# Kernel tuning notes

Measured on AMD Instinct MI355X. Metric: run time of the kernel, lower is better.

The kernel has to match this reference:

```python
import jax, jax.numpy as jnp
import numpy as np
import math

N_HEADS, INPUT_DIM, EMBED_DIM = 8, 512, 512
KEY_DIM = EMBED_DIM // N_HEADS  # val_dim == key_dim == 64
B, NQ, G = 4, 2048, 2048


def setup_inputs() -> dict:
    key = jax.random.key(0)
    ks = jax.random.split(key, 7)
    stdv_k = 1.0 / math.sqrt(KEY_DIM)
    stdv_e = 1.0 / math.sqrt(EMBED_DIM)
    return {
        "q": jax.random.normal(ks[0], (B, NQ, INPUT_DIM), jnp.float32),
        "h": jax.random.normal(ks[1], (B, G, INPUT_DIM), jnp.float32),
        "mask": jax.random.randint(ks[2], (B, NQ, G), 0, 2) == 1,  # True = attention not possible
        "W_query": jax.random.uniform(ks[3], (N_HEADS, INPUT_DIM, KEY_DIM), jnp.float32, -stdv_k, stdv_k),
        "W_key": jax.random.uniform(ks[4], (N_HEADS, INPUT_DIM, KEY_DIM), jnp.float32, -stdv_k, stdv_k),
        "W_val": jax.random.uniform(ks[5], (N_HEADS, INPUT_DIM, KEY_DIM), jnp.float32, -stdv_k, stdv_k),
        "W_out": jax.random.uniform(ks[6], (N_HEADS, KEY_DIM, EMBED_DIM), jnp.float32, -stdv_e, stdv_e),
    }


def reference(q, h, mask, W_query, W_key, W_val, W_out):
    norm = 1.0 / math.sqrt(KEY_DIM)
    # Per-head projections: (H, B, S, kd)
    Q = jnp.einsum("bqd,hdk->hbqk", q, W_query)
    K = jnp.einsum("bgd,hdk->hbgk", h, W_key)
    V = jnp.einsum("bgd,hdv->hbgv", h, W_val)
    # Full attention scores: (H, B, NQ, G)
    comp = norm * jnp.einsum("hbqk,hbgk->hbqg", Q, K)
    m = mask[None]  # (1, B, NQ, G) broadcasts over heads
    comp = jnp.where(m, -jnp.inf, comp)
    attn = jax.nn.softmax(comp, axis=-1)
    attn = jnp.where(m, 0.0, attn)  # mirrors the clone + zero step (also fixes all-masked rows)
    heads = jnp.einsum("hbqg,hbgv->hbqv", attn, V)
    # Output projection: flatten heads and apply W_out (H, vd, E)
    out = jnp.einsum("hbqv,hve->bqe", heads, W_out)
    return out
```

## Files before the change

### kernel.cpp

```cpp
#include <hip/hip_runtime.h>
#include <hip/hip_bf16.h>
#include <stdint.h>

#define NHEADS 8
#define INDIM 512
#define EMB 512
#define BSZ 4
#define NQS 2048
#define GS 2048

#define ALPHA_F 0.18033688011112042f

#if __has_builtin(__builtin_amdgcn_exp2f)
#define EXP2(x) __builtin_amdgcn_exp2f(x)
#else
#define EXP2(x) __expf((x)*0.69314718056f)
#endif

typedef short bf16x8 __attribute__((ext_vector_type(8)));
typedef float f32x4 __attribute__((ext_vector_type(4)));
typedef float f32x16 __attribute__((ext_vector_type(16)));
typedef unsigned int u32x4 __attribute__((ext_vector_type(4)));

static __device__ __forceinline__ unsigned short f2bf(float f) {
  unsigned int u = __builtin_bit_cast(unsigned int, f);
  unsigned int rounding = 0x7FFFu + ((u >> 16) & 1u);
  u += rounding;
  return (unsigned short)(u >> 16);
}

typedef __attribute__((address_space(3))) void lds_void;
typedef __attribute__((address_space(1))) const void gm_void;
static __device__ __forceinline__ void gll16(const void* g, void* s) {
  __builtin_amdgcn_global_load_lds((gm_void*)g, (lds_void*)s, 16, 0, 0);
}

__global__ void k_prep(const float4* __restrict__ q, const float4* __restrict__ h,
                       const void* __restrict__ mask,
                       const float* __restrict__ wq, const float* __restrict__ wk,
                       const float* __restrict__ wv, const float* __restrict__ wo,
                       ushort4* __restrict__ qb, ushort4* __restrict__ hb,
                       unsigned short* __restrict__ wqt, unsigned short* __restrict__ wkvt,
                       unsigned short* __restrict__ wot, unsigned short* __restrict__ maskB16) {
  int blk = blockIdx.x, t = threadIdx.x;
  if (blk < 2048) {
    const float4* src = blk < 1024 ? q : h;
    ushort4* dst = blk < 1024 ? qb : hb;
    int base = (blk & 1023) * 256 + t;
#pragma unroll
    for (int i = 0; i < 4; i++) {
      int idx = base + i * 262144;
      float4 v = src[idx];
      ushort4 o;
      o.x = f2bf(v.x); o.y = f2bf(v.y); o.z = f2bf(v.z); o.w = f2bf(v.w);
      dst[idx] = o;
    }
  } else if (blk < 3072) {
    const unsigned int* m32h = (const unsigned int*)mask;
    bool bytes = __ballot(m32h[t & 63] > 1u) != 0ull;
    int base = (blk - 2048) * 256 + t;
#pragma unroll
    for (int i = 0; i < 4; i++) {
      int widx = base + i * 262144;
      unsigned int bits = 0;
      if (bytes) {
        const uchar4* p = (const uchar4*)((const unsigned char*)mask + (size_t)widx * 16);
#pragma unroll
        for (int j = 0; j < 4; j++) {
          uchar4 v = p[j];
          bits |= ((v.x ? 1u : 0u) << (4 * j)) | ((v.y ? 1u : 0u) << (4 * j + 1)) |
                  ((v.z ? 1u : 0u) << (4 * j + 2)) | ((v.w ? 1u : 0u) << (4 * j + 3));
        }
      } else {
        const int4* p = (const int4*)((const int*)mask + (size_t)widx * 16);
#pragma unroll
        for (int j = 0; j < 4; j++) {
          int4 v = p[j];
          bits |= ((v.x ? 1u : 0u) << (4 * j)) | ((v.y ? 1u : 0u) << (4 * j + 1)) |
                  ((v.z ? 1u : 0u) << (4 * j + 2)) | ((v.w ? 1u : 0u) << (4 * j + 3));
        }
      }
      maskB16[widx] = (unsigned short)bits;
    }
  } else {
    int id = (blk - 3072) * 256 + t;
#pragma unroll
    for (int i = 0; i < 8; i++) {
      int e = id * 8 + i;
      int which = e >> 18, r = e & 262143;
      int k = r & 511, n = r >> 9;
      int hh = n >> 6, j = n & 63;
      if (which == 0) wqt[r] = f2bf(wq[hh * 32768 + k * 64 + j] * ALPHA_F);
      else if (which == 1) wkvt[r] = f2bf(wk[hh * 32768 + k * 64 + j]);
      else if (which == 2) wkvt[262144 + r] = f2bf(wv[hh * 32768 + k * 64 + j]);
      else wot[r] = f2bf(wo[k * 512 + n]);
    }
  }
}

template <int MODE>
__global__ __launch_bounds__(256) void k_gemm3(const unsigned short* __restrict__ A,
                                               const unsigned short* __restrict__ Bt,
                                               void* __restrict__ C, void* __restrict__ C2) {
  __shared__ unsigned short As[2][4096];
  __shared__ unsigned short Bs[2][8192];
  int m0 = blockIdx.x * 64, n0 = blockIdx.y * 128;
  int t = threadIdx.x;
  int w = t >> 6, l = t & 63, c = l & 15, lg = l >> 4;
  int wr = w >> 1, wc = w & 1;

  int rbA = t >> 7, kcc = (t >> 4) & 7, cc = t & 15;
  const unsigned short* aG = A + (size_t)(m0 + rbA * 16 + cc) * 512 + kcc * 8;
  const unsigned short* bG = Bt + (size_t)(n0 + rbA * 16 + cc) * 512 + kcc * 8;
  int ldsOff = w * 1024 + (t & 63) * 16;

  f32x4 acc[2][4];
#pragma unroll
  for (int mi = 0; mi < 2; mi++)
#pragma unroll
    for (int ni = 0; ni < 4; ni++) acc[mi][ni] = {0.f, 0.f, 0.f, 0.f};

  gll16(aG, (char*)As[0] + ldsOff);
  gll16(aG + 32 * 512, (char*)As[0] + ldsOff + 4096);
  gll16(bG, (char*)Bs[0] + ldsOff);
  gll16(bG + 32 * 512, (char*)Bs[0] + ldsOff + 4096);
  gll16(bG + 64 * 512, (char*)Bs[0] + ldsOff + 8192);
  gll16(bG + 96 * 512, (char*)Bs[0] + ldsOff + 12288);

  for (int kk = 0; kk < 8; kk++) {
    int cur = kk & 1;
    asm volatile("s_waitcnt vmcnt(0)" ::: "memory");
    __builtin_amdgcn_s_barrier();
    if (kk < 7) {
      int ko = (kk + 1) * 64;
      gll16(aG + ko, (char*)As[cur ^ 1] + ldsOff);
      gll16(aG + ko + 32 * 512, (char*)As[cur ^ 1] + ldsOff + 4096);
      gll16(bG + ko, (char*)Bs[cur ^ 1] + ldsOff);
      gll16(bG + ko + 32 * 512, (char*)Bs[cur ^ 1] + ldsOff + 4096);
      gll16(bG + ko + 64 * 512, (char*)Bs[cur ^ 1] + ldsOff + 8192);
      gll16(bG + ko + 96 * 512, (char*)Bs[cur ^ 1] + ldsOff + 12288);
    }
    bf16x8 af[2][2], bfr[4][2];
#pragma unroll
    for (int kc = 0; kc < 2; kc++) {
#pragma unroll
      for (int mi = 0; mi < 2; mi++)
        af[mi][kc] = *(const bf16x8*)((const char*)As[cur] + ((wr * 2 + mi) * 128 + (kc * 4 + lg) * 16 + c) * 16);
#pragma unroll
      for (int ni = 0; ni < 4; ni++)
        bfr[ni][kc] = *(const bf16x8*)((const char*)Bs[cur] + ((wc * 4 + ni) * 128 + (kc * 4 + lg) * 16 + c) * 16);
    }
#pragma unroll
    for (int kc = 0; kc < 2; kc++)
#pragma unroll
      for (int mi = 0; mi < 2; mi++)
#pragma unroll
        for (int ni = 0; ni < 4; ni++)
          acc[mi][ni] = __builtin_amdgcn_mfma_f32_16x16x32_bf16(af[mi][kc], bfr[ni][kc], acc[mi][ni], 0, 0, 0);
  }

#pragma unroll
  for (int mi = 0; mi < 2; mi++)
#pragma unroll
    for (int ni = 0; ni < 4; ni++) {
      int row = m0 + wr * 32 + mi * 16 + 4 * lg;
      int col = n0 + wc * 64 + ni * 16 + c;
#pragma unroll
      for (int r = 0; r < 4; r++)
        ((float*)C)[(size_t)(row + r) * 512 + col] = acc[mi][ni][r];
    }
}

__global__ __launch_bounds__(256) void k_gemmQKV2(const unsigned short* __restrict__ qb_,
                                                  const unsigned short* __restrict__ hb_,
                                                  const unsigned short* __restrict__ wqt,
                                                  const unsigned short* __restrict__ wkvt,
                                                  unsigned short* __restrict__ Qp,
                                                  unsigned short* __restrict__ Kp,
                                                  unsigned short* __restrict__ Vt) {
  __shared__ unsigned short As[2][4096];
  __shared__ unsigned short Bs[2][4096];
  int ny = blockIdx.y;
  const unsigned short* A = (ny < 4) ? qb_ : hb_;
  const unsigned short* Bt = (ny < 4) ? wqt : wkvt;
  int n0 = (ny < 4) ? ny * 128 : (ny - 4) * 128;
  int m0 = blockIdx.x * 128;
  int t = threadIdx.x;
  int w = t >> 6, l = t & 63, c = l & 15, lg = l >> 4;
  int wr = w >> 1, wc = w & 1;

  int sRow = (t >> 6) * 16 + (t & 15);
  int sK = ((t >> 4) & 3) * 8;
  const unsigned short* aG = A + (size_t)(m0 + sRow) * 512 + sK;
  const unsigned short* bG = Bt + (size_t)(n0 + sRow) * 512 + sK;
  int ldsOff = t * 16;

  f32x4 acc[4][4];
#pragma unroll
  for (int mi = 0; mi < 4; mi++)
#pragma unroll
    for (int ni = 0; ni < 4; ni++) acc[mi][ni] = {0.f, 0.f, 0.f, 0.f};

  gll16(aG, (char*)As[0] + ldsOff);
  gll16(aG + 64 * 512, (char*)As[0] + ldsOff + 4096);
  gll16(bG, (char*)Bs[0] + ldsOff);
  gll16(bG + 64 * 512, (char*)Bs[0] + ldsOff + 4096);

  for (int kk = 0; kk < 16; kk++) {
    int cur = kk & 1;
    asm volatile("s_waitcnt vmcnt(0)" ::: "memory");
    __builtin_amdgcn_s_barrier();
    if (kk < 15) {
      int ko = (kk + 1) * 32;
      gll16(aG + ko, (char*)As[cur ^ 1] + ldsOff);
      gll16(aG + ko + 64 * 512, (char*)As[cur ^ 1] + ldsOff + 4096);
      gll16(bG + ko, (char*)Bs[cur ^ 1] + ldsOff);
      gll16(bG + ko + 64 * 512, (char*)Bs[cur ^ 1] + ldsOff + 4096);
    }
    bf16x8 af[4], bfr[4];
#pragma unroll
    for (int mi = 0; mi < 4; mi++)
      af[mi] = *(const bf16x8*)((const char*)As[cur] + (((wr * 4 + mi) * 64 + l) * 16));
#pragma unroll
    for (int ni = 0; ni < 4; ni++)
      bfr[ni] = *(const bf16x8*)((const char*)Bs[cur] + (((wc * 4 + ni) * 64 + l) * 16));
#pragma unroll
    for (int mi = 0; mi < 4; mi++)
#pragma unroll
      for (int ni = 0; ni < 4; ni++)
        acc[mi][ni] = __builtin_amdgcn_mfma_f32_16x16x32_bf16(af[mi], bfr[ni], acc[mi][ni], 0, 0, 0);
  }

#pragma unroll
  for (int mi = 0; mi < 4; mi++)
#pragma unroll
    for (int ni = 0; ni < 4; ni++) {
      int row = m0 + wr * 64 + mi * 16 + 4 * lg;
      int col = n0 + wc * 64 + ni * 16 + c;
      if (ny < 4) {
#pragma unroll
        for (int r = 0; r < 4; r++)
          Qp[(size_t)(row + r) * 512 + col] = f2bf(acc[mi][ni][r]);
      } else if (col < 512) {
#pragma unroll
        for (int r = 0; r < 4; r++)
          Kp[(size_t)(row + r) * 512 + col] = f2bf(acc[mi][ni][r]);
      } else {
        int col5 = col - 512, hd2 = col5 >> 6, vv = col5 & 63;
        int bb = row >> 11, g = row & 2047;
        ushort4 u;
        u.x = f2bf(acc[mi][ni][0]);
        u.y = f2bf(acc[mi][ni][1]);
        u.z = f2bf(acc[mi][ni][2]);
        u.w = f2bf(acc[mi][ni][3]);
        *(ushort4*)(Vt + (size_t)((bb * 8 + hd2) * 64 + vv) * GS + g) = u;
      }
    }
}

__global__ __launch_bounds__(256, 2) void k_attn8(const unsigned short* __restrict__ Qp,
                                                  const unsigned short* __restrict__ Kp,
                                                  const unsigned short* __restrict__ Vt,
                                                  const unsigned short* __restrict__ maskB16,
                                                  unsigned short* __restrict__ Hd) {
  __shared__ unsigned short Ksh[2][4096];
  __shared__ unsigned short Vsh[2][4096];

  int bid = blockIdx.x;
  int fid = (bid & 7) * 64 + (bid >> 3);
  int qtile = fid & 15;
  int bh = fid >> 4;
  int b = bh >> 3, hd = bh & 7;

  int t = threadIdx.x;
  int w = t >> 6, l = t & 63;
  int lo = l & 31, hi = l >> 5, hi4 = hi * 4;
  int q = qtile * 128 + w * 32 + lo;

  const unsigned short* qrow = Qp + (size_t)(b * NQS + q) * 512 + hd * 64 + hi * 8;
  bf16x8 qf[4];
#pragma unroll
  for (int s = 0; s < 4; s++) qf[s] = *(const bf16x8*)(qrow + s * 16);

  const unsigned short* kg0 = Kp + (size_t)(b * GS + lo) * 512 + hd * 64 + w * 16 + hi * 8;
  int vbS = (t >> 7) & 1, s2S = (t >> 6) & 1;
  const unsigned short* vg0 = Vt + (size_t)(bh * 64 + vbS * 32 + lo) * GS + s2S * 16 + hi * 8;
  char* kd[2] = {(char*)Ksh[0] + w * 1024, (char*)Ksh[1] + w * 1024};
  char* vd[2] = {(char*)Vsh[0] + w * 1024, (char*)Vsh[1] + w * 1024};

  f32x16 o0, o1;
#pragma unroll
  for (int i = 0; i < 16; i++) { o0[i] = 0.f; o1[i] = 0.f; }
  float ls[4] = {0.f, 0.f, 0.f, 0.f};

  const unsigned long long* mrow = (const unsigned long long*)maskB16 + (size_t)(b * NQS + q) * 32;

  gll16(kg0, kd[0]);
  gll16(kg0 + 32 * 512, kd[0] + 4096);
  gll16(vg0, vd[0]);
  gll16(vg0 + 32, vd[0] + 4096);
  unsigned long long wm = mrow[0], wmn = 0;

  for (int kt = 0; kt < 32; kt++) {
    int cur = kt & 1;
    asm volatile("s_waitcnt vmcnt(0)" ::: "memory");
    __builtin_amdgcn_s_barrier();
    if (kt < 31) {
      const unsigned short* kg = kg0 + (size_t)(kt + 1) * 64 * 512;
      const unsigned short* vg = vg0 + (size_t)(kt + 1) * 64;
      gll16(kg, kd[cur ^ 1]);
      gll16(kg + 32 * 512, kd[cur ^ 1] + 4096);
      gll16(vg, vd[cur ^ 1]);
      gll16(vg + 32, vd[cur ^ 1] + 4096);
      wmn = mrow[kt + 1];
    }

#pragma unroll
    for (int g2 = 0; g2 < 2; g2++) {
      const unsigned short* Kc = (const unsigned short*)Ksh[cur] + g2 * 2048;
      f32x16 sreg;
#pragma unroll
      for (int i = 0; i < 16; i++) sreg[i] = 0.f;
      __builtin_amdgcn_s_setprio(1);
#pragma unroll
      for (int s = 0; s < 4; s++) {
        bf16x8 ka = *(const bf16x8*)(Kc + (s * 64 + l) * 8);
        sreg = __builtin_amdgcn_mfma_f32_32x32x16_bf16(ka, qf[s], sreg, 0, 0, 0);
      }
      __builtin_amdgcn_s_setprio(0);
      unsigned int mbits = (unsigned int)(wm >> (g2 * 32));
      float p[16];
#pragma unroll
      for (int r = 0; r < 16; r++) {
        float e = EXP2(sreg[r]);
        unsigned bit = (mbits >> ((r & 3) + 8 * (r >> 2) + hi4)) & 1u;
        p[r] = bit ? 0.f : e;
        ls[r & 3] += p[r];
      }
      unsigned int cw0, cw1, cw2, cw3, cw4, cw5, cw6, cw7;
      asm("v_cvt_pk_bf16_f32 %0, %1, %2" : "=v"(cw0) : "v"(p[0]), "v"(p[1]));
      asm("v_cvt_pk_bf16_f32 %0, %1, %2" : "=v"(cw1) : "v"(p[2]), "v"(p[3]));
      asm("v_cvt_pk_bf16_f32 %0, %1, %2" : "=v"(cw2) : "v"(p[4]), "v"(p[5]));
      asm("v_cvt_pk_bf16_f32 %0, %1, %2" : "=v"(cw3) : "v"(p[6]), "v"(p[7]));
      asm("v_cvt_pk_bf16_f32 %0, %1, %2" : "=v"(cw4) : "v"(p[8]), "v"(p[9]));
      asm("v_cvt_pk_bf16_f32 %0, %1, %2" : "=v"(cw5) : "v"(p[10]), "v"(p[11]));
      asm("v_cvt_pk_bf16_f32 %0, %1, %2" : "=v"(cw6) : "v"(p[12]), "v"(p[13]));
      asm("v_cvt_pk_bf16_f32 %0, %1, %2" : "=v"(cw7) : "v"(p[14]), "v"(p[15]));
      asm("v_permlane32_swap_b32 %0, %1" : "+v"(cw0), "+v"(cw2));
      asm("v_permlane32_swap_b32 %0, %1" : "+v"(cw1), "+v"(cw3));
      asm("v_permlane32_swap_b32 %0, %1" : "+v"(cw4), "+v"(cw6));
      asm("v_permlane32_swap_b32 %0, %1" : "+v"(cw5), "+v"(cw7));
      u32x4 pw0 = {cw0, cw1, cw2, cw3};
      u32x4 pw1 = {cw4, cw5, cw6, cw7};
      bf16x8 pb0 = __builtin_bit_cast(bf16x8, pw0);
      bf16x8 pb1 = __builtin_bit_cast(bf16x8, pw1);
      const unsigned short* Vc = (const unsigned short*)Vsh[cur] + g2 * 2048;
      bf16x8 va00 = *(const bf16x8*)(Vc + (0 * 64 + l) * 8);
      bf16x8 va01 = *(const bf16x8*)(Vc + (1 * 64 + l) * 8);
      bf16x8 va10 = *(const bf16x8*)(Vc + (2 * 64 + l) * 8);
      bf16x8 va11 = *(const bf16x8*)(Vc + (3 * 64 + l) * 8);
      __builtin_amdgcn_s_setprio(1);
      o0 = __builtin_amdgcn_mfma_f32_32x32x16_bf16(va00, pb0, o0, 0, 0, 0);
      o1 = __builtin_amdgcn_mfma_f32_32x32x16_bf16(va10, pb0, o1, 0, 0, 0);
      o0 = __builtin_amdgcn_mfma_f32_32x32x16_bf16(va01, pb1, o0, 0, 0, 0);
      o1 = __builtin_amdgcn_mfma_f32_32x32x16_bf16(va11, pb1, o1, 0, 0, 0);
      __builtin_amdgcn_s_setprio(0);
    }
    wm = wmn;
  }

  float lsum = (ls[0] + ls[1]) + (ls[2] + ls[3]);
  lsum += __shfl_xor(lsum, 32);
  float inv = lsum > 0.f ? 1.0f / lsum : 0.f;
  unsigned short* hrow = Hd + (size_t)(b * NQS + q) * 512 + hd * 64;
#pragma unroll
  for (int vt = 0; vt < 2; vt++) {
#pragma unroll
    for (int gr = 0; gr < 4; gr++) {
      ushort4 u;
      float v0 = (vt ? o1[gr * 4 + 0] : o0[gr * 4 + 0]) * inv;
      float v1 = (vt ? o1[gr * 4 + 1] : o0[gr * 4 + 1]) * inv;
      float v2 = (vt ? o1[gr * 4 + 2] : o0[gr * 4 + 2]) * inv;
      float v3 = (vt ? o1[gr * 4 + 3] : o0[gr * 4 + 3]) * inv;
      u.x = f2bf(v0); u.y = f2bf(v1); u.z = f2bf(v2); u.w = f2bf(v3);
      int vv = vt * 32 + 8 * gr + hi4;
      *(ushort4*)(hrow + vv) = u;
    }
  }
}


extern "C" void kernel_launch(void* const* d_in, const int* in_sizes, int n_in,
                              void* d_out, int out_size, void* d_ws, size_t ws_size,
                              hipStream_t stream) {
  const float* q = (const float*)d_in[0];
  const float* h = (const float*)d_in[1];
  const void* mask = d_in[2];
  const float* wq = (const float*)d_in[3];
  const float* wk = (const float*)d_in[4];
  const float* wv = (const float*)d_in[5];
  const float* wo = (const float*)d_in[6];
  float* out = (float*)d_out;

  unsigned short* qb_ = (unsigned short*)d_ws;
  unsigned short* hb_ = qb_ + 8192 * 512;
  unsigned short* Qp = hb_ + 8192 * 512;
  unsigned short* Kp = Qp + 8192 * 512;
  unsigned short* Vtp = Kp + 8192 * 512;
  unsigned short* Hd = Vtp + 8192 * 512;
  unsigned short* wqt = Hd + 8192 * 512;
  unsigned short* wkvt = wqt + 512 * 512;
  unsigned short* wot = wkvt + 1024 * 512;
  unsigned short* maskB16 = wot + 512 * 512;

  k_prep<<<3584, 256, 0, stream>>>((const float4*)q, (const float4*)h, mask, wq, wk, wv, wo,
                                   (ushort4*)qb_, (ushort4*)hb_, wqt, wkvt, wot, maskB16);
  dim3 gqkv(64, 12);
  k_gemmQKV2<<<gqkv, 256, 0, stream>>>(qb_, hb_, wqt, wkvt, Qp, Kp, Vtp);
  k_attn8<<<512, 256, 0, stream>>>(Qp, Kp, Vtp, maskB16, Hd);
  dim3 go(128, 4);
  k_gemm3<1><<<go, 256, 0, stream>>>(Hd, wot, out, nullptr);
}
```

Measured before the change: 133.0 us.

## Issue both QK^T MFMA groups upfront in attention; retile output GEMM to 128x128

The attention inner loop now computes both 32-key score blocks' MFMAs back to back before running softmax and PV on each. This lets the second score MFMA chain overlap the first block's exp and pack work, at the cost of an extra 16-float accumulator in registers. The output projection GEMM is replaced with a 128x128 tile using a 32-wide K step and a simpler LDS layout, so each block does more MFMAs per load and fewer blocks are launched.

After: 132.7 us. About the same (-0.2%).

```diff
diff --git a/kernel.cpp b/kernel.cpp
--- a/kernel.cpp
+++ b/kernel.cpp
@@ -98,78 +98,6 @@
   }
 }
 
-template <int MODE>
-__global__ __launch_bounds__(256) void k_gemm3(const unsigned short* __restrict__ A,
-                                               const unsigned short* __restrict__ Bt,
-                                               void* __restrict__ C, void* __restrict__ C2) {
-  __shared__ unsigned short As[2][4096];
-  __shared__ unsigned short Bs[2][8192];
-  int m0 = blockIdx.x * 64, n0 = blockIdx.y * 128;
-  int t = threadIdx.x;
-  int w = t >> 6, l = t & 63, c = l & 15, lg = l >> 4;
-  int wr = w >> 1, wc = w & 1;
-
-  int rbA = t >> 7, kcc = (t >> 4) & 7, cc = t & 15;
-  const unsigned short* aG = A + (size_t)(m0 + rbA * 16 + cc) * 512 + kcc * 8;
-  const unsigned short* bG = Bt + (size_t)(n0 + rbA * 16 + cc) * 512 + kcc * 8;
-  int ldsOff = w * 1024 + (t & 63) * 16;
-
-  f32x4 acc[2][4];
-#pragma unroll
-  for (int mi = 0; mi < 2; mi++)
-#pragma unroll
-    for (int ni = 0; ni < 4; ni++) acc[mi][ni] = {0.f, 0.f, 0.f, 0.f};
-
-  gll16(aG, (char*)As[0] + ldsOff);
-  gll16(aG + 32 * 512, (char*)As[0] + ldsOff + 4096);
-  gll16(bG, (char*)Bs[0] + ldsOff);
-  gll16(bG + 32 * 512, (char*)Bs[0] + ldsOff + 4096);
-  gll16(bG + 64 * 512, (char*)Bs[0] + ldsOff + 8192);
-  gll16(bG + 96 * 512, (char*)Bs[0] + ldsOff + 12288);
-
-  for (int kk = 0; kk < 8; kk++) {
-    int cur = kk & 1;
-    asm volatile("s_waitcnt vmcnt(0)" ::: "memory");
-    __builtin_amdgcn_s_barrier();
-    if (kk < 7) {
-      int ko = (kk + 1) * 64;
-      gll16(aG + ko, (char*)As[cur ^ 1] + ldsOff);
-      gll16(aG + ko + 32 * 512, (char*)As[cur ^ 1] + ldsOff + 4096);
-      gll16(bG + ko, (char*)Bs[cur ^ 1] + ldsOff);
-      gll16(bG + ko + 32 * 512, (char*)Bs[cur ^ 1] + ldsOff + 4096);
-      gll16(bG + ko + 64 * 512, (char*)Bs[cur ^ 1] + ldsOff + 8192);
-      gll16(bG + ko + 96 * 512, (char*)Bs[cur ^ 1] + ldsOff + 12288);
-    }
-    bf16x8 af[2][2], bfr[4][2];
-#pragma unroll
-    for (int kc = 0; kc < 2; kc++) {
-#pragma unroll
-      for (int mi = 0; mi < 2; mi++)
-        af[mi][kc] = *(const bf16x8*)((const char*)As[cur] + ((wr * 2 + mi) * 128 + (kc * 4 + lg) * 16 + c) * 16);
-#pragma unroll
-      for (int ni = 0; ni < 4; ni++)
-        bfr[ni][kc] = *(const bf16x8*)((const char*)Bs[cur] + ((wc * 4 + ni) * 128 + (kc * 4 + lg) * 16 + c) * 16);
-    }
-#pragma unroll
-    for (int kc = 0; kc < 2; kc++)
-#pragma unroll
-      for (int mi = 0; mi < 2; mi++)
-#pragma unroll
-        for (int ni = 0; ni < 4; ni++)
-          acc[mi][ni] = __builtin_amdgcn_mfma_f32_16x16x32_bf16(af[mi][kc], bfr[ni][kc], acc[mi][ni], 0, 0, 0);
-  }
-
-#pragma unroll
-  for (int mi = 0; mi < 2; mi++)
-#pragma unroll
-    for (int ni = 0; ni < 4; ni++) {
-      int row = m0 + wr * 32 + mi * 16 + 4 * lg;
-      int col = n0 + wc * 64 + ni * 16 + c;
-#pragma unroll
-      for (int r = 0; r < 4; r++)
-        ((float*)C)[(size_t)(row + r) * 512 + col] = acc[mi][ni][r];
-    }
-}
 
 __global__ __launch_bounds__(256) void k_gemmQKV2(const unsigned short* __restrict__ qb_,
                                                   const unsigned short* __restrict__ hb_,
@@ -258,11 +186,75 @@
     }
 }
 
-__global__ __launch_bounds__(256, 2) void k_attn8(const unsigned short* __restrict__ Qp,
-                                                  const unsigned short* __restrict__ Kp,
-                                                  const unsigned short* __restrict__ Vt,
-                                                  const unsigned short* __restrict__ maskB16,
-                                                  unsigned short* __restrict__ Hd) {
+__global__ __launch_bounds__(256) void k_gemmO(const unsigned short* __restrict__ A,
+                                               const unsigned short* __restrict__ Bt,
+                                               float* __restrict__ C) {
+  __shared__ unsigned short As[2][4096];
+  __shared__ unsigned short Bs[2][4096];
+  int m0 = blockIdx.x * 128, n0 = blockIdx.y * 128;
+  int t = threadIdx.x;
+  int w = t >> 6, l = t & 63, c = l & 15, lg = l >> 4;
+  int wr = w >> 1, wc = w & 1;
+
+  int sRow = (t >> 6) * 16 + (t & 15);
+  int sK = ((t >> 4) & 3) * 8;
+  const unsigned short* aG = A + (size_t)(m0 + sRow) * 512 + sK;
+  const unsigned short* bG = Bt + (size_t)(n0 + sRow) * 512 + sK;
+  int ldsOff = t * 16;
+
+  f32x4 acc[4][4];
+#pragma unroll
+  for (int mi = 0; mi < 4; mi++)
+#pragma unroll
+    for (int ni = 0; ni < 4; ni++) acc[mi][ni] = {0.f, 0.f, 0.f, 0.f};
+
+  gll16(aG, (char*)As[0] + ldsOff);
+  gll16(aG + 64 * 512, (char*)As[0] + ldsOff + 4096);
+  gll16(bG, (char*)Bs[0] + ldsOff);
+  gll16(bG + 64 * 512, (char*)Bs[0] + ldsOff + 4096);
+
+  for (int kk = 0; kk < 16; kk++) {
+    int cur = kk & 1;
+    asm volatile("s_waitcnt vmcnt(0)" ::: "memory");
+    __builtin_amdgcn_s_barrier();
+    if (kk < 15) {
+      int ko = (kk + 1) * 32;
+      gll16(aG + ko, (char*)As[cur ^ 1] + ldsOff);
+      gll16(aG + ko + 64 * 512, (char*)As[cur ^ 1] + ldsOff + 4096);
+      gll16(bG + ko, (char*)Bs[cur ^ 1] + ldsOff);
+      gll16(bG + ko + 64 * 512, (char*)Bs[cur ^ 1] + ldsOff + 4096);
+    }
+    bf16x8 af[4], bfr[4];
+#pragma unroll
+    for (int mi = 0; mi < 4; mi++)
+      af[mi] = *(const bf16x8*)((const char*)As[cur] + (((wr * 4 + mi) * 64 + l) * 16));
+#pragma unroll
+    for (int ni = 0; ni < 4; ni++)
+      bfr[ni] = *(const bf16x8*)((const char*)Bs[cur] + (((wc * 4 + ni) * 64 + l) * 16));
+#pragma unroll
+    for (int mi = 0; mi < 4; mi++)
+#pragma unroll
+      for (int ni = 0; ni < 4; ni++)
+        acc[mi][ni] = __builtin_amdgcn_mfma_f32_16x16x32_bf16(af[mi], bfr[ni], acc[mi][ni], 0, 0, 0);
+  }
+
+#pragma unroll
+  for (int mi = 0; mi < 4; mi++)
+#pragma unroll
+    for (int ni = 0; ni < 4; ni++) {
+      int row = m0 + wr * 64 + mi * 16 + 4 * lg;
+      int col = n0 + wc * 64 + ni * 16 + c;
+#pragma unroll
+      for (int r = 0; r < 4; r++)
+        C[(size_t)(row + r) * 512 + col] = acc[mi][ni][r];
+    }
+}
+
+__global__ __launch_bounds__(256, 2) void k_attn10(const unsigned short* __restrict__ Qp,
+                                                   const unsigned short* __restrict__ Kp,
+                                                   const unsigned short* __restrict__ Vt,
+                                                   const unsigned short* __restrict__ maskB16,
+                                                   unsigned short* __restrict__ Hd) {
   __shared__ unsigned short Ksh[2][4096];
   __shared__ unsigned short Vsh[2][4096];
 
@@ -315,55 +307,100 @@
       wmn = mrow[kt + 1];
     }
 
-#pragma unroll
-    for (int g2 = 0; g2 < 2; g2++) {
-      const unsigned short* Kc = (const unsigned short*)Ksh[cur] + g2 * 2048;
-      f32x16 sreg;
-#pragma unroll
-      for (int i = 0; i < 16; i++) sreg[i] = 0.f;
-      __builtin_amdgcn_s_setprio(1);
-#pragma unroll
-      for (int s = 0; s < 4; s++) {
-        bf16x8 ka = *(const bf16x8*)(Kc + (s * 64 + l) * 8);
-        sreg = __builtin_amdgcn_mfma_f32_32x32x16_bf16(ka, qf[s], sreg, 0, 0, 0);
-      }
-      __builtin_amdgcn_s_setprio(0);
-      unsigned int mbits = (unsigned int)(wm >> (g2 * 32));
-      float p[16];
-#pragma unroll
-      for (int r = 0; r < 16; r++) {
-        float e = EXP2(sreg[r]);
-        unsigned bit = (mbits >> ((r & 3) + 8 * (r >> 2) + hi4)) & 1u;
-        p[r] = bit ? 0.f : e;
-        ls[r & 3] += p[r];
-      }
-      unsigned int cw0, cw1, cw2, cw3, cw4, cw5, cw6, cw7;
-      asm("v_cvt_pk_bf16_f32 %0, %1, %2" : "=v"(cw0) : "v"(p[0]), "v"(p[1]));
-      asm("v_cvt_pk_bf16_f32 %0, %1, %2" : "=v"(cw1) : "v"(p[2]), "v"(p[3]));
-      asm("v_cvt_pk_bf16_f32 %0, %1, %2" : "=v"(cw2) : "v"(p[4]), "v"(p[5]));
-      asm("v_cvt_pk_bf16_f32 %0, %1, %2" : "=v"(cw3) : "v"(p[6]), "v"(p[7]));
-      asm("v_cvt_pk_bf16_f32 %0, %1, %2" : "=v"(cw4) : "v"(p[8]), "v"(p[9]));
-      asm("v_cvt_pk_bf16_f32 %0, %1, %2" : "=v"(cw5) : "v"(p[10]), "v"(p[11]));
-      asm("v_cvt_pk_bf16_f32 %0, %1, %2" : "=v"(cw6) : "v"(p[12]), "v"(p[13]));
-      asm("v_cvt_pk_bf16_f32 %0, %1, %2" : "=v"(cw7) : "v"(p[14]), "v"(p[15]));
-      asm("v_permlane32_swap_b32 %0, %1" : "+v"(cw0), "+v"(cw2));
-      asm("v_permlane32_swap_b32 %0, %1" : "+v"(cw1), "+v"(cw3));
-      asm("v_permlane32_swap_b32 %0, %1" : "+v"(cw4), "+v"(cw6));
-      asm("v_permlane32_swap_b32 %0, %1" : "+v"(cw5), "+v"(cw7));
-      u32x4 pw0 = {cw0, cw1, cw2, cw3};
-      u32x4 pw1 = {cw4, cw5, cw6, cw7};
-      bf16x8 pb0 = __builtin_bit_cast(bf16x8, pw0);
-      bf16x8 pb1 = __builtin_bit_cast(bf16x8, pw1);
-      const unsigned short* Vc = (const unsigned short*)Vsh[cur] + g2 * 2048;
+    const unsigned short* Kc = (const unsigned short*)Ksh[cur];
+    const unsigned short* Vc = (const unsigned short*)Vsh[cur];
+
+    f32x16 s0, s1;
+#pragma unroll
+    for (int i = 0; i < 16; i++) { s0[i] = 0.f; s1[i] = 0.f; }
+    __builtin_amdgcn_s_setprio(1);
+#pragma unroll
+    for (int s = 0; s < 4; s++) {
+      bf16x8 ka0 = *(const bf16x8*)(Kc + (s * 64 + l) * 8);
+      s0 = __builtin_amdgcn_mfma_f32_32x32x16_bf16(ka0, qf[s], s0, 0, 0, 0);
+    }
+#pragma unroll
+    for (int s = 0; s < 4; s++) {
+      bf16x8 ka1 = *(const bf16x8*)(Kc + 2048 + (s * 64 + l) * 8);
+      s1 = __builtin_amdgcn_mfma_f32_32x32x16_bf16(ka1, qf[s], s1, 0, 0, 0);
+    }
+    __builtin_amdgcn_s_setprio(0);
+
+    unsigned int mb0 = (unsigned int)wm;
+    float p0[16];
+#pragma unroll
+    for (int r = 0; r < 16; r++) {
+      float e = EXP2(s0[r]);
+      unsigned bit = (mb0 >> ((r & 3) + 8 * (r >> 2) + hi4)) & 1u;
+      p0[r] = bit ? 0.f : e;
+      ls[r & 3] += p0[r];
+    }
+    unsigned int a0, a1, a2, a3, a4, a5, a6, a7;
+    asm("v_cvt_pk_bf16_f32 %0, %1, %2" : "=v"(a0) : "v"(p0[0]), "v"(p0[1]));
+    asm("v_cvt_pk_bf16_f32 %0, %1, %2" : "=v"(a1) : "v"(p0[2]), "v"(p0[3]));
+    asm("v_cvt_pk_bf16_f32 %0, %1, %2" : "=v"(a2) : "v"(p0[4]), "v"(p0[5]));
+    asm("v_cvt_pk_bf16_f32 %0, %1, %2" : "=v"(a3) : "v"(p0[6]), "v"(p0[7]));
+    asm("v_cvt_pk_bf16_f32 %0, %1, %2" : "=v"(a4) : "v"(p0[8]), "v"(p0[9]));
+    asm("v_cvt_pk_bf16_f32 %0, %1, %2" : "=v"(a5) : "v"(p0[10]), "v"(p0[11]));
+    asm("v_cvt_pk_bf16_f32 %0, %1, %2" : "=v"(a6) : "v"(p0[12]), "v"(p0[13]));
+    asm("v_cvt_pk_bf16_f32 %0, %1, %2" : "=v"(a7) : "v"(p0[14]), "v"(p0[15]));
+    asm("v_permlane32_swap_b32 %0, %1" : "+v"(a0), "+v"(a2));
+    asm("v_permlane32_swap_b32 %0, %1" : "+v"(a1), "+v"(a3));
+    asm("v_permlane32_swap_b32 %0, %1" : "+v"(a4), "+v"(a6));
+    asm("v_permlane32_swap_b32 %0, %1" : "+v"(a5), "+v"(a7));
+    u32x4 pw00 = {a0, a1, a2, a3};
+    u32x4 pw01 = {a4, a5, a6, a7};
+    bf16x8 pb00 = __builtin_bit_cast(bf16x8, pw00);
+    bf16x8 pb01 = __builtin_bit_cast(bf16x8, pw01);
+    {
       bf16x8 va00 = *(const bf16x8*)(Vc + (0 * 64 + l) * 8);
       bf16x8 va01 = *(const bf16x8*)(Vc + (1 * 64 + l) * 8);
       bf16x8 va10 = *(const bf16x8*)(Vc + (2 * 64 + l) * 8);
       bf16x8 va11 = *(const bf16x8*)(Vc + (3 * 64 + l) * 8);
       __builtin_amdgcn_s_setprio(1);
-      o0 = __builtin_amdgcn_mfma_f32_32x32x16_bf16(va00, pb0, o0, 0, 0, 0);
-      o1 = __builtin_amdgcn_mfma_f32_32x32x16_bf16(va10, pb0, o1, 0, 0, 0);
-      o0 = __builtin_amdgcn_mfma_f32_32x32x16_bf16(va01, pb1, o0, 0, 0, 0);
-      o1 = __builtin_amdgcn_mfma_f32_32x32x16_bf16(va11, pb1, o1, 0, 0, 0);
+      o0 = __builtin_amdgcn_mfma_f32_32x32x16_bf16(va00, pb00, o0, 0, 0, 0);
+      o1 = __builtin_amdgcn_mfma_f32_32x32x16_bf16(va10, pb00, o1, 0, 0, 0);
+      o0 = __builtin_amdgcn_mfma_f32_32x32x16_bf16(va01, pb01, o0, 0, 0, 0);
+      o1 = __builtin_amdgcn_mfma_f32_32x32x16_bf16(va11, pb01, o1, 0, 0, 0);
+      __builtin_amdgcn_s_setprio(0);
+    }
+
+    unsigned int mb1 = (unsigned int)(wm >> 32);
+    float p1[16];
+#pragma unroll
+    for (int r = 0; r < 16; r++) {
+      float e = EXP2(s1[r]);
+      unsigned bit = (mb1 >> ((r & 3) + 8 * (r >> 2) + hi4)) & 1u;
+      p1[r] = bit ? 0.f : e;
+      ls[r & 3] += p1[r];
+    }
+    unsigned int b0, b1, b2, b3, b4, b5, b6, b7;
+    asm("v_cvt_pk_bf16_f32 %0, %1, %2" : "=v"(b0) : "v"(p1[0]), "v"(p1[1]));
+    asm("v_cvt_pk_bf16_f32 %0, %1, %2" : "=v"(b1) : "v"(p1[2]), "v"(p1[3]));
+    asm("v_cvt_pk_bf16_f32 %0, %1, %2" : "=v"(b2) : "v"(p1[4]), "v"(p1[5]));
+    asm("v_cvt_pk_bf16_f32 %0, %1, %2" : "=v"(b3) : "v"(p1[6]), "v"(p1[7]));
+    asm("v_cvt_pk_bf16_f32 %0, %1, %2" : "=v"(b4) : "v"(p1[8]), "v"(p1[9]));
+    asm("v_cvt_pk_bf16_f32 %0, %1, %2" : "=v"(b5) : "v"(p1[10]), "v"(p1[11]));
+    asm("v_cvt_pk_bf16_f32 %0, %1, %2" : "=v"(b6) : "v"(p1[12]), "v"(p1[13]));
+    asm("v_cvt_pk_bf16_f32 %0, %1, %2" : "=v"(b7) : "v"(p1[14]), "v"(p1[15]));
+    asm("v_permlane32_swap_b32 %0, %1" : "+v"(b0), "+v"(b2));
+    asm("v_permlane32_swap_b32 %0, %1" : "+v"(b1), "+v"(b3));
+    asm("v_permlane32_swap_b32 %0, %1" : "+v"(b4), "+v"(b6));
+    asm("v_permlane32_swap_b32 %0, %1" : "+v"(b5), "+v"(b7));
+    u32x4 pw10 = {b0, b1, b2, b3};
+    u32x4 pw11 = {b4, b5, b6, b7};
+    bf16x8 pb10 = __builtin_bit_cast(bf16x8, pw10);
+    bf16x8 pb11 = __builtin_bit_cast(bf16x8, pw11);
+    {
+      bf16x8 vb00 = *(const bf16x8*)(Vc + 2048 + (0 * 64 + l) * 8);
+      bf16x8 vb01 = *(const bf16x8*)(Vc + 2048 + (1 * 64 + l) * 8);
+      bf16x8 vb10 = *(const bf16x8*)(Vc + 2048 + (2 * 64 + l) * 8);
+      bf16x8 vb11 = *(const bf16x8*)(Vc + 2048 + (3 * 64 + l) * 8);
+      __builtin_amdgcn_s_setprio(1);
+      o0 = __builtin_amdgcn_mfma_f32_32x32x16_bf16(vb00, pb10, o0, 0, 0, 0);
+      o1 = __builtin_amdgcn_mfma_f32_32x32x16_bf16(vb10, pb10, o1, 0, 0, 0);
+      o0 = __builtin_amdgcn_mfma_f32_32x32x16_bf16(vb01, pb11, o0, 0, 0, 0);
+      o1 = __builtin_amdgcn_mfma_f32_32x32x16_bf16(vb11, pb11, o1, 0, 0, 0);
       __builtin_amdgcn_s_setprio(0);
     }
     wm = wmn;
@@ -417,7 +454,7 @@
                                    (ushort4*)qb_, (ushort4*)hb_, wqt, wkvt, wot, maskB16);
   dim3 gqkv(64, 12);
   k_gemmQKV2<<<gqkv, 256, 0, stream>>>(qb_, hb_, wqt, wkvt, Qp, Kp, Vtp);
-  k_attn8<<<512, 256, 0, stream>>>(Qp, Kp, Vtp, maskB16, Hd);
-  dim3 go(128, 4);
-  k_gemm3<1><<<go, 256, 0, stream>>>(Hd, wot, out, nullptr);
-}
+  k_attn10<<<512, 256, 0, stream>>>(Qp, Kp, Vtp, maskB16, Hd);
+  dim3 go(64, 4);
+  k_gemmO<<<go, 256, 0, stream>>>(Hd, wot, out);
+}
```
